# Kernel optimization log

Hardware: AMD Instinct MI355X
Metric: run time of the kernel (lower is better)

The kernel has to match this reference:

```python
import jax, jax.numpy as jnp
import numpy as np

N_NODES = 50000
NEG_SLOPE = 0.2


def gat_layer(x, src, dst, w_src, w_dst, att_src, att_dst, bias):
    """Single-head PyG-style GATConv (bipartite weights, same x for src/dst)."""
    xs = x @ w_src                      # [N, C] messages (source projection)
    xd = x @ w_dst                      # [N, C] destination projection
    a_s = xs @ att_src                  # [N] per-node src attention logit
    a_d = xd @ att_dst                  # [N] per-node dst attention logit
    e = jax.nn.leaky_relu(a_s[src] + a_d[dst], NEG_SLOPE)   # [E]
    # segment softmax over edges grouped by destination node
    m = jax.ops.segment_max(e, dst, num_segments=N_NODES)    # [N]
    ex = jnp.exp(e - m[dst])
    denom = jax.ops.segment_sum(ex, dst, num_segments=N_NODES)  # [N]
    alpha = ex / denom[dst]             # [E]
    out = jax.ops.segment_sum(alpha[:, None] * xs[src], dst, num_segments=N_NODES)
    return out + bias


def setup_inputs() -> dict:
    key = jax.random.key(0)
    ks = jax.random.split(key, 12)
    d_in, hid, out = 256, 128, 128
    inv = lambda d: 1.0 / np.sqrt(d)
    x = jax.random.normal(ks[0], (N_NODES, d_in), dtype=jnp.float32)
    edge_index = jax.random.randint(ks[1], (2, 800000), 0, N_NODES, dtype=jnp.int32)
    return {
        "x": x,
        "edge_index": edge_index,
        "w1_src": jax.random.normal(ks[2], (d_in, hid), jnp.float32) * inv(d_in),
        "w1_dst": jax.random.normal(ks[3], (d_in, hid), jnp.float32) * inv(d_in),
        "att1_src": jax.random.normal(ks[4], (hid,), jnp.float32) * inv(hid),
        "att1_dst": jax.random.normal(ks[5], (hid,), jnp.float32) * inv(hid),
        "b1": jnp.zeros((hid,), jnp.float32),
        "w2_src": jax.random.normal(ks[6], (hid, out), jnp.float32) * inv(hid),
        "w2_dst": jax.random.normal(ks[7], (hid, out), jnp.float32) * inv(hid),
        "att2_src": jax.random.normal(ks[8], (out,), jnp.float32) * inv(out),
        "att2_dst": jax.random.normal(ks[9], (out,), jnp.float32) * inv(out),
        "b2": jnp.zeros((out,), jnp.float32),
    }


def reference(x, edge_index, w1_src, w1_dst, att1_src, att1_dst, b1,
              w2_src, w2_dst, att2_src, att2_dst, b2):
    # add self loops once (GATConv default add_self_loops=True)
    loop = jnp.arange(N_NODES, dtype=edge_index.dtype)
    src = jnp.concatenate([edge_index[0], loop])
    dst = jnp.concatenate([edge_index[1], loop])
    h = gat_layer(x, src, dst, w1_src, w1_dst, att1_src, att1_dst, b1)
    h = jax.nn.relu(h)
    return gat_layer(h, src, dst, w2_src, w2_dst, att2_src, att2_dst, b2)
```

## Files before the change

kernel.cpp:

```cpp
#include <hip/hip_runtime.h>

#define NN 50000
#define MAXD 64
#define NEG_SLOPE 0.2f

typedef _Float16 half8 __attribute__((ext_vector_type(8)));
typedef _Float16 half2v __attribute__((ext_vector_type(2)));
typedef float floatx4 __attribute__((ext_vector_type(4)));


__global__ __launch_bounds__(256) void mega_kernel(
    const int* __restrict__ src, const int* __restrict__ dst,
    int* cnt, int* seg, int e, int G_SCAT,
    const float* __restrict__ w1s, const float* __restrict__ a1s,
    const float* __restrict__ w1d, const float* __restrict__ a1d,
    const float* __restrict__ w2s, const float* __restrict__ a2s,
    const float* __restrict__ w2d, const float* __restrict__ a2d,
    float* u1, float* v1, float* u2, float* v2,
    const float* __restrict__ x, _Float16* __restrict__ C, int M, int G_GEMM) {
  constexpr int K = 256, KP = 72;
  __shared__ _Float16 Bt[128 * KP];
  int bid = blockIdx.x, tid = threadIdx.x;
  if (bid < G_SCAT) {
    int i0 = (bid * 256 + tid) * 8;
    int total = e + NN;
#pragma unroll
    for (int j = 0; j < 8; ++j) {
      int i = i0 + j;
      if (i < total) {
        int d, s;
        if (i < e) { d = dst[i]; s = src[i]; }
        else       { d = i - e;  s = d; }
        int r = atomicAdd(&cnt[d], 1);
        if (r < MAXD) seg[(size_t)d * MAXD + r] = s;
      }
    }
  } else if (bid < G_SCAT + 4) {
    int b = bid - G_SCAT;
    const float *w, *a;
    float* o;
    int d;
    if (b == 0) { w = w1s; a = a1s; o = u1; d = K; }
    else if (b == 1) { w = w1d; a = a1d; o = v1; d = K; }
    else if (b == 2) { w = w2s; a = a2s; o = u2; d = 128; }
    else { w = w2d; a = a2d; o = v2; d = 128; }
    if (tid < d) {
      float s = 0.f;
      for (int j = 0; j < 128; ++j) s += w[tid * 128 + j] * a[j];
      o[tid] = s;
    }
  } else {
    __builtin_amdgcn_s_setprio(1);
    int gb = bid - G_SCAT - 4;
    int lane = tid & 63, wave = tid >> 6;
    int row_base = gb * 64 + wave * 16;
    int lr = lane & 15, lk = lane >> 4;
    floatx4 acc[8];
#pragma unroll
    for (int q = 0; q < 8; ++q) acc[q] = {0.f, 0.f, 0.f, 0.f};
    for (int kc = 0; kc < K; kc += 64) {
      for (int idx = tid; idx < 128 * 64; idx += 256) {
        int k = idx >> 7, c = idx & 127;
        Bt[c * KP + k] = (_Float16)w1s[(size_t)(kc + k) * 128 + c];
      }
      __syncthreads();
#pragma unroll
      for (int k0 = 0; k0 < 64; k0 += 32) {
        int row = row_base + lr;
        half8 a = {0, 0, 0, 0, 0, 0, 0, 0};
        if (row < M) {
          const float* ap = x + (size_t)row * K + kc + k0 + lk * 8;
          float4 f0 = *reinterpret_cast<const float4*>(ap);
          float4 f1 = *reinterpret_cast<const float4*>(ap + 4);
          a = half8{(_Float16)f0.x, (_Float16)f0.y, (_Float16)f0.z, (_Float16)f0.w,
                    (_Float16)f1.x, (_Float16)f1.y, (_Float16)f1.z, (_Float16)f1.w};
        }
        half8 b[8];
#pragma unroll
        for (int q = 0; q < 8; ++q)
          b[q] = *reinterpret_cast<const half8*>(&Bt[(q * 16 + lr) * KP + k0 + lk * 8]);
#pragma unroll
        for (int q = 0; q < 8; ++q)
          acc[q] = __builtin_amdgcn_mfma_f32_16x16x32_f16(a, b[q], acc[q], 0, 0, 0);
      }
      __syncthreads();
    }
#pragma unroll
    for (int q = 0; q < 8; ++q)
#pragma unroll
      for (int r = 0; r < 4; ++r) {
        int row = row_base + lk * 4 + r;
        if (row < M) C[(size_t)row * 128 + q * 16 + lr] = (_Float16)acc[q][r];
      }
    __builtin_amdgcn_s_setprio(0);
  }
}

__global__ __launch_bounds__(256) void ls_kernel(
    const int* __restrict__ cnt, int* seg, int G_SORT,
    const float* __restrict__ x, const float* __restrict__ u,
    const float* __restrict__ v, float* a_s, float* a_d) {
  int bid = blockIdx.x, tid = threadIdx.x;
  if (bid < G_SORT) {
    int wid = bid * 4 + (tid >> 6);
    int lane = tid & 63;
    if (wid < NN) {
      int L = cnt[wid];
      L = L < MAXD ? L : MAXD;
      if (L > 1) {
        int* srow = seg + (size_t)wid * MAXD;
        int v2_ = (lane < L) ? srow[lane] : 0x7fffffff;
#pragma unroll
        for (int k = 2; k <= 64; k <<= 1) {
#pragma unroll
          for (int j = k >> 1; j > 0; j >>= 1) {
            int other = __shfl_xor(v2_, j);
            bool dir = ((lane & k) == 0);
            bool lower = ((lane & j) == 0);
            int mn = v2_ < other ? v2_ : other;
            int mx = v2_ < other ? other : v2_;
            v2_ = (dir == lower) ? mn : mx;
          }
        }
        if (lane < L) srow[lane] = v2_;
      }
    }
  } else {
    int wid = (bid - G_SORT) * 4 + (tid >> 6);
    int lane = tid & 63;
    if (wid >= NN) return;
    const float* xr = x + (size_t)wid * 256 + lane * 4;
    float4 xv = *reinterpret_cast<const float4*>(xr);
    float4 uu = *reinterpret_cast<const float4*>(u + lane * 4);
    float4 vv = *reinterpret_cast<const float4*>(v + lane * 4);
    float s1 = xv.x * uu.x + xv.y * uu.y + xv.z * uu.z + xv.w * uu.w;
    float s2 = xv.x * vv.x + xv.y * vv.y + xv.z * vv.z + xv.w * vv.w;
#pragma unroll
    for (int off = 32; off; off >>= 1) {
      s1 += __shfl_xor(s1, off);
      s2 += __shfl_xor(s2, off);
    }
    if (lane == 0) { a_s[wid] = s1; a_d[wid] = s2; }
  }
}

__global__ __launch_bounds__(256) void fused2_kernel(
    const _Float16* __restrict__ A, const float* __restrict__ B,
    _Float16* __restrict__ C, int M, int G_GEMM,
    const _Float16* __restrict__ xin, const float* __restrict__ u,
    const float* __restrict__ v, float* a_s, float* a_d) {
  constexpr int K = 128, KP = 72;
  __shared__ _Float16 Bt[128 * KP];
  int bid = blockIdx.x, tid = threadIdx.x;
  if (bid < G_GEMM) {
    __builtin_amdgcn_s_setprio(1);
    int lane = tid & 63, wave = tid >> 6;
    int row_base = bid * 64 + wave * 16;
    int lr = lane & 15, lk = lane >> 4;
    floatx4 acc[8];
#pragma unroll
    for (int q = 0; q < 8; ++q) acc[q] = {0.f, 0.f, 0.f, 0.f};
    for (int kc = 0; kc < K; kc += 64) {
      for (int idx = tid; idx < 128 * 64; idx += 256) {
        int k = idx >> 7, c = idx & 127;
        Bt[c * KP + k] = (_Float16)B[(size_t)(kc + k) * 128 + c];
      }
      __syncthreads();
#pragma unroll
      for (int k0 = 0; k0 < 64; k0 += 32) {
        int row = row_base + lr;
        half8 a = {0, 0, 0, 0, 0, 0, 0, 0};
        if (row < M) a = *reinterpret_cast<const half8*>(&A[(size_t)row * K + kc + k0 + lk * 8]);
        half8 b[8];
#pragma unroll
        for (int q = 0; q < 8; ++q)
          b[q] = *reinterpret_cast<const half8*>(&Bt[(q * 16 + lr) * KP + k0 + lk * 8]);
#pragma unroll
        for (int q = 0; q < 8; ++q)
          acc[q] = __builtin_amdgcn_mfma_f32_16x16x32_f16(a, b[q], acc[q], 0, 0, 0);
      }
      __syncthreads();
    }
#pragma unroll
    for (int q = 0; q < 8; ++q)
#pragma unroll
      for (int r = 0; r < 4; ++r) {
        int row = row_base + lk * 4 + r;
        if (row < M) C[(size_t)row * 128 + q * 16 + lr] = (_Float16)acc[q][r];
      }
    __builtin_amdgcn_s_setprio(0);
  } else {
    int wid = (bid - G_GEMM) * 4 + (tid >> 6);
    int lane = tid & 63;
    if (wid >= NN) return;
    float s1 = 0.f, s2 = 0.f;
    const half2v* xr = reinterpret_cast<const half2v*>(&xin[(size_t)wid * 128]);
    {
      int i = lane;
      half2v xv = xr[i];
      float x0 = (float)xv[0], x1 = (float)xv[1];
      s1 = x0 * u[2 * i] + x1 * u[2 * i + 1];
      s2 = x0 * v[2 * i] + x1 * v[2 * i + 1];
    }
#pragma unroll
    for (int off = 32; off; off >>= 1) {
      s1 += __shfl_xor(s1, off);
      s2 += __shfl_xor(s2, off);
    }
    if (lane == 0) { a_s[wid] = s1; a_d[wid] = s2; }
  }
}

template <int LAYER>
__global__ __launch_bounds__(256) void agg_kernel(const int* __restrict__ cnt,
                                                  const int* __restrict__ seg,
                                                  const float* __restrict__ a_s,
                                                  const float* __restrict__ a_d,
                                                  const _Float16* __restrict__ xs,
                                                  const float* __restrict__ bias,
                                                  void* __restrict__ outp, int n) {
  int wid = (blockIdx.x * blockDim.x + threadIdx.x) >> 6;
  int lane = threadIdx.x & 63;
  if (wid >= n) return;
  int g = lane >> 3, lr = lane & 7;
  int L = cnt[wid];
  L = L < MAXD ? L : MAXD;
  const int* srow = seg + (size_t)wid * MAXD;
  float ad = a_d[wid];

  float denom = 0.f;
  float acc[16];
#pragma unroll
  for (int j = 0; j < 16; ++j) acc[j] = 0.f;

  int i = g;
  int s_cur = (i < L) ? srow[i] : -1;
  int i2 = i + 8;
  int s_next = (i2 < L) ? srow[i2] : -1;
  half8 v_cur0, v_cur1;
  float as_cur = 0.f;
  if (s_cur >= 0) {
    const _Float16* pr = &xs[(size_t)s_cur * 128 + lr * 16];
    v_cur0 = *reinterpret_cast<const half8*>(pr);
    v_cur1 = *reinterpret_cast<const half8*>(pr + 8);
    as_cur = a_s[s_cur];
  }
  while (s_cur >= 0) {
    half8 v_nx0, v_nx1;
    float as_nx = 0.f;
    if (s_next >= 0) {
      const _Float16* pr = &xs[(size_t)s_next * 128 + lr * 16];
      v_nx0 = *reinterpret_cast<const half8*>(pr);
      v_nx1 = *reinterpret_cast<const half8*>(pr + 8);
      as_nx = a_s[s_next];
    }
    int i3 = i2 + 8;
    int s_nx2 = (i3 < L) ? srow[i3] : -1;

    float e = as_cur + ad;
    e = e > 0.f ? e : NEG_SLOPE * e;
    float w = __expf(e);
    denom += w;
#pragma unroll
    for (int j = 0; j < 8; ++j) {
      acc[j] += w * (float)v_cur0[j];
      acc[8 + j] += w * (float)v_cur1[j];
    }
    s_cur = s_next; v_cur0 = v_nx0; v_cur1 = v_nx1; as_cur = as_nx;
    s_next = s_nx2; i2 = i3;
  }
  denom += __shfl_xor(denom, 8);
  denom += __shfl_xor(denom, 16);
  denom += __shfl_xor(denom, 32);
#pragma unroll
  for (int j = 0; j < 16; ++j) {
    acc[j] += __shfl_xor(acc[j], 8);
    acc[j] += __shfl_xor(acc[j], 16);
    acc[j] += __shfl_xor(acc[j], 32);
  }
  if (g == 0) {
    float inv = 1.0f / denom;
    float o[16];
#pragma unroll
    for (int j = 0; j < 16; ++j) o[j] = acc[j] * inv + bias[lr * 16 + j];
    if (LAYER == 1) {
      half8 h0, h1;
#pragma unroll
      for (int j = 0; j < 8; ++j) {
        h0[j] = (_Float16)fmaxf(o[j], 0.f);
        h1[j] = (_Float16)fmaxf(o[8 + j], 0.f);
      }
      _Float16* op = &((_Float16*)outp)[(size_t)wid * 128 + lr * 16];
      *reinterpret_cast<half8*>(op) = h0;
      *reinterpret_cast<half8*>(op + 8) = h1;
    } else {
      float* op = &((float*)outp)[(size_t)wid * 128 + lr * 16];
#pragma unroll
      for (int q = 0; q < 4; ++q) {
        float4 f = make_float4(o[q * 4], o[q * 4 + 1], o[q * 4 + 2], o[q * 4 + 3]);
        *reinterpret_cast<float4*>(op + q * 4) = f;
      }
    }
  }
}

extern "C" void kernel_launch(void* const* d_in, const int* in_sizes, int n_in,
                              void* d_out, int out_size, void* d_ws, size_t ws_size,
                              hipStream_t stream) {
  const float* x        = (const float*)d_in[0];
  const int*   eidx     = (const int*)d_in[1];
  const float* w1_src   = (const float*)d_in[2];
  const float* w1_dst   = (const float*)d_in[3];
  const float* att1_src = (const float*)d_in[4];
  const float* att1_dst = (const float*)d_in[5];
  const float* b1       = (const float*)d_in[6];
  const float* w2_src   = (const float*)d_in[7];
  const float* w2_dst   = (const float*)d_in[8];
  const float* att2_src = (const float*)d_in[9];
  const float* att2_dst = (const float*)d_in[10];
  const float* b2       = (const float*)d_in[11];

  const int E = in_sizes[1] / 2;
  const int* src = eidx;
  const int* dst = eidx + E;

  _Float16* h_h = (_Float16*)d_out;
  float*    out = (float*)d_out;

  char* ws = (char*)d_ws;
  size_t off = 0;
  auto alloc = [&](size_t bytes) -> void* {
    void* p = ws + off;
    off = (off + bytes + 255) & ~(size_t)255;
    return p;
  };
  _Float16* xs_h = (_Float16*)alloc((size_t)NN * 128 * sizeof(_Float16));
  float* a_s     = (float*)alloc((size_t)NN * sizeof(float));
  float* a_d     = (float*)alloc((size_t)NN * sizeof(float));
  int*   cnt     = (int*)alloc((size_t)NN * sizeof(int));
  int*   seg     = (int*)alloc((size_t)NN * MAXD * sizeof(int));
  float* u1      = (float*)alloc(256 * sizeof(float));
  float* v1      = (float*)alloc(256 * sizeof(float));
  float* u2      = (float*)alloc(256 * sizeof(float));
  float* v2      = (float*)alloc(256 * sizeof(float));

  const int G_SCAT = ((E + NN) / 8 + 255) / 256;
  const int G_GEMM = (NN + 63) / 64;
  const int G_SORT = (NN + 3) / 4;
  const int G_LOG  = (NN + 3) / 4;
  const int wave_blocks = (NN * 64 + 255) / 256;

  hipMemsetAsync(cnt, 0, NN * sizeof(int), stream);

  mega_kernel<<<G_SCAT + 4 + G_GEMM, 256, 0, stream>>>(
      src, dst, cnt, seg, E, G_SCAT,
      w1_src, att1_src, w1_dst, att1_dst, w2_src, att2_src, w2_dst, att2_dst,
      u1, v1, u2, v2, x, xs_h, NN, G_GEMM);

  ls_kernel<<<G_SORT + G_LOG, 256, 0, stream>>>(cnt, seg, G_SORT, x, u1, v1, a_s, a_d);

  agg_kernel<1><<<wave_blocks, 256, 0, stream>>>(cnt, seg, a_s, a_d, xs_h, b1, h_h, NN);

  fused2_kernel<<<G_GEMM + G_LOG, 256, 0, stream>>>(
      h_h, w2_src, xs_h, NN, G_GEMM, h_h, u2, v2, a_s, a_d);

  agg_kernel<2><<<wave_blocks, 256, 0, stream>>>(cnt, seg, a_s, a_d, xs_h, b2, out, NN);
}
```

Before: 165.9 us.

## Fuse per-row sort into layer-1 aggregation and logits into mega kernel

Moves the attention-vector precompute and the cnt zeroing into a small init kernel that replaces the memset. The layer-1 logit dot products now run as extra blocks of the scatter/GEMM mega kernel. The bitonic sort of each destination's source list now happens inside the layer-1 aggregation wave, which keeps the sorted indices in registers and reads them by shuffle. This removes one launch and one pass over seg, at the cost of an extra launch for init and sort work on the aggregation critical path. It also drops the setprio hint on the GEMM blocks.

```diff
diff --git a/kernel.cpp b/kernel.cpp
--- a/kernel.cpp
+++ b/kernel.cpp
@@ -8,15 +8,39 @@
 typedef _Float16 half2v __attribute__((ext_vector_type(2)));
 typedef float floatx4 __attribute__((ext_vector_type(4)));
 
-
-__global__ __launch_bounds__(256) void mega_kernel(
-    const int* __restrict__ src, const int* __restrict__ dst,
-    int* cnt, int* seg, int e, int G_SCAT,
+__global__ __launch_bounds__(256) void init_kernel(
     const float* __restrict__ w1s, const float* __restrict__ a1s,
     const float* __restrict__ w1d, const float* __restrict__ a1d,
     const float* __restrict__ w2s, const float* __restrict__ a2s,
     const float* __restrict__ w2d, const float* __restrict__ a2d,
-    float* u1, float* v1, float* u2, float* v2,
+    float* u1, float* v1, float* u2, float* v2, int din, int* cnt) {
+  int b = blockIdx.x, tid = threadIdx.x;
+  if (b < 4) {
+    const float *w, *a;
+    float* o;
+    int d;
+    if (b == 0) { w = w1s; a = a1s; o = u1; d = din; }
+    else if (b == 1) { w = w1d; a = a1d; o = v1; d = din; }
+    else if (b == 2) { w = w2s; a = a2s; o = u2; d = 128; }
+    else { w = w2d; a = a2d; o = v2; d = 128; }
+    if (tid < d) {
+      float s = 0.f;
+      for (int j = 0; j < 128; ++j) s += w[tid * 128 + j] * a[j];
+      o[tid] = s;
+    }
+  } else {
+    int i = (b - 4) * 256 + tid;
+    if (i < NN) cnt[i] = 0;
+  }
+}
+
+
+__global__ __launch_bounds__(256) void mega_kernel(
+    const int* __restrict__ src, const int* __restrict__ dst,
+    int* cnt, int* seg, int e, int G_SCAT,
+    const float* __restrict__ w1s,
+    const float* __restrict__ u1, const float* __restrict__ v1,
+    float* a_s, float* a_d,
     const float* __restrict__ x, _Float16* __restrict__ C, int M, int G_GEMM) {
   constexpr int K = 256, KP = 72;
   __shared__ _Float16 Bt[128 * KP];
@@ -35,23 +59,8 @@
         if (r < MAXD) seg[(size_t)d * MAXD + r] = s;
       }
     }
-  } else if (bid < G_SCAT + 4) {
-    int b = bid - G_SCAT;
-    const float *w, *a;
-    float* o;
-    int d;
-    if (b == 0) { w = w1s; a = a1s; o = u1; d = K; }
-    else if (b == 1) { w = w1d; a = a1d; o = v1; d = K; }
-    else if (b == 2) { w = w2s; a = a2s; o = u2; d = 128; }
-    else { w = w2d; a = a2d; o = v2; d = 128; }
-    if (tid < d) {
-      float s = 0.f;
-      for (int j = 0; j < 128; ++j) s += w[tid * 128 + j] * a[j];
-      o[tid] = s;
-    }
-  } else {
-    __builtin_amdgcn_s_setprio(1);
-    int gb = bid - G_SCAT - 4;
+  } else if (bid < G_SCAT + G_GEMM) {
+    int gb = bid - G_SCAT;
     int lane = tid & 63, wave = tid >> 6;
     int row_base = gb * 64 + wave * 16;
     int lr = lane & 15, lk = lane >> 4;
@@ -92,47 +101,14 @@
         int row = row_base + lk * 4 + r;
         if (row < M) C[(size_t)row * 128 + q * 16 + lr] = (_Float16)acc[q][r];
       }
-    __builtin_amdgcn_s_setprio(0);
-  }
-}
-
-__global__ __launch_bounds__(256) void ls_kernel(
-    const int* __restrict__ cnt, int* seg, int G_SORT,
-    const float* __restrict__ x, const float* __restrict__ u,
-    const float* __restrict__ v, float* a_s, float* a_d) {
-  int bid = blockIdx.x, tid = threadIdx.x;
-  if (bid < G_SORT) {
-    int wid = bid * 4 + (tid >> 6);
-    int lane = tid & 63;
-    if (wid < NN) {
-      int L = cnt[wid];
-      L = L < MAXD ? L : MAXD;
-      if (L > 1) {
-        int* srow = seg + (size_t)wid * MAXD;
-        int v2_ = (lane < L) ? srow[lane] : 0x7fffffff;
-#pragma unroll
-        for (int k = 2; k <= 64; k <<= 1) {
-#pragma unroll
-          for (int j = k >> 1; j > 0; j >>= 1) {
-            int other = __shfl_xor(v2_, j);
-            bool dir = ((lane & k) == 0);
-            bool lower = ((lane & j) == 0);
-            int mn = v2_ < other ? v2_ : other;
-            int mx = v2_ < other ? other : v2_;
-            v2_ = (dir == lower) ? mn : mx;
-          }
-        }
-        if (lane < L) srow[lane] = v2_;
-      }
-    }
   } else {
-    int wid = (bid - G_SORT) * 4 + (tid >> 6);
+    int wid = (bid - G_SCAT - G_GEMM) * 4 + (tid >> 6);
     int lane = tid & 63;
     if (wid >= NN) return;
     const float* xr = x + (size_t)wid * 256 + lane * 4;
     float4 xv = *reinterpret_cast<const float4*>(xr);
-    float4 uu = *reinterpret_cast<const float4*>(u + lane * 4);
-    float4 vv = *reinterpret_cast<const float4*>(v + lane * 4);
+    float4 uu = *reinterpret_cast<const float4*>(u1 + lane * 4);
+    float4 vv = *reinterpret_cast<const float4*>(v1 + lane * 4);
     float s1 = xv.x * uu.x + xv.y * uu.y + xv.z * uu.z + xv.w * uu.w;
     float s2 = xv.x * vv.x + xv.y * vv.y + xv.z * vv.z + xv.w * vv.w;
 #pragma unroll
@@ -141,6 +117,106 @@
       s2 += __shfl_xor(s2, off);
     }
     if (lane == 0) { a_s[wid] = s1; a_d[wid] = s2; }
+  }
+}
+
+__global__ __launch_bounds__(256) void agg1_kernel(
+    const int* __restrict__ cnt, int* __restrict__ seg,
+    const float* __restrict__ a_s, const float* __restrict__ a_d,
+    const _Float16* __restrict__ xs, const float* __restrict__ bias,
+    _Float16* __restrict__ outp, int n) {
+  int wid = (blockIdx.x * blockDim.x + threadIdx.x) >> 6;
+  int lane = threadIdx.x & 63;
+  if (wid >= n) return;
+  int L = cnt[wid];
+  L = L < MAXD ? L : MAXD;
+  int* srow = seg + (size_t)wid * MAXD;
+
+  int v = (lane < L) ? srow[lane] : 0x7fffffff;
+#pragma unroll
+  for (int k = 2; k <= 64; k <<= 1) {
+#pragma unroll
+    for (int j = k >> 1; j > 0; j >>= 1) {
+      int other = __shfl_xor(v, j);
+      bool dir = ((lane & k) == 0);
+      bool lower = ((lane & j) == 0);
+      int mn = v < other ? v : other;
+      int mx = v < other ? other : v;
+      v = (dir == lower) ? mn : mx;
+    }
+  }
+  if (lane < L) srow[lane] = v;
+
+  int g = lane >> 3, lr = lane & 7;
+  float ad = a_d[wid];
+  float denom = 0.f;
+  float acc[16];
+#pragma unroll
+  for (int j = 0; j < 16; ++j) acc[j] = 0.f;
+
+  auto idx_at = [&](int s_) -> int {
+    int val = __shfl(v, s_ & 63);
+    return (s_ < L) ? val : -1;
+  };
+
+  int slot = g;
+  int s_cur = idx_at(slot);
+  int slot2 = slot + 8;
+  int s_next = idx_at(slot2);
+  half8 c0, c1;
+  float as_c = 0.f;
+  if (s_cur >= 0) {
+    const _Float16* pr = &xs[(size_t)s_cur * 128 + lr * 16];
+    c0 = *reinterpret_cast<const half8*>(pr);
+    c1 = *reinterpret_cast<const half8*>(pr + 8);
+    as_c = a_s[s_cur];
+  }
+  while (s_cur >= 0) {
+    half8 n0, n1;
+    float as_n = 0.f;
+    if (s_next >= 0) {
+      const _Float16* pr = &xs[(size_t)s_next * 128 + lr * 16];
+      n0 = *reinterpret_cast<const half8*>(pr);
+      n1 = *reinterpret_cast<const half8*>(pr + 8);
+      as_n = a_s[s_next];
+    }
+    int slot3 = slot2 + 8;
+    int s_nx2 = idx_at(slot3);
+
+    float e = as_c + ad;
+    e = e > 0.f ? e : NEG_SLOPE * e;
+    float w = __expf(e);
+    denom += w;
+#pragma unroll
+    for (int j = 0; j < 8; ++j) {
+      acc[j] += w * (float)c0[j];
+      acc[8 + j] += w * (float)c1[j];
+    }
+    s_cur = s_next; c0 = n0; c1 = n1; as_c = as_n;
+    s_next = s_nx2; slot2 = slot3;
+  }
+  denom += __shfl_xor(denom, 8);
+  denom += __shfl_xor(denom, 16);
+  denom += __shfl_xor(denom, 32);
+#pragma unroll
+  for (int j = 0; j < 16; ++j) {
+    acc[j] += __shfl_xor(acc[j], 8);
+    acc[j] += __shfl_xor(acc[j], 16);
+    acc[j] += __shfl_xor(acc[j], 32);
+  }
+  if (g == 0) {
+    float inv = 1.0f / denom;
+    half8 h0, h1;
+#pragma unroll
+    for (int j = 0; j < 8; ++j) {
+      float o0 = acc[j] * inv + bias[lr * 16 + j];
+      float o1 = acc[8 + j] * inv + bias[lr * 16 + 8 + j];
+      h0[j] = (_Float16)fmaxf(o0, 0.f);
+      h1[j] = (_Float16)fmaxf(o1, 0.f);
+    }
+    _Float16* op = &outp[(size_t)wid * 128 + lr * 16];
+    *reinterpret_cast<half8*>(op) = h0;
+    *reinterpret_cast<half8*>(op + 8) = h1;
   }
 }
 
@@ -193,7 +269,7 @@
     int wid = (bid - G_GEMM) * 4 + (tid >> 6);
     int lane = tid & 63;
     if (wid >= NN) return;
-    float s1 = 0.f, s2 = 0.f;
+    float s1, s2;
     const half2v* xr = reinterpret_cast<const half2v*>(&xin[(size_t)wid * 128]);
     {
       int i = lane;
@@ -211,14 +287,11 @@
   }
 }
 
-template <int LAYER>
-__global__ __launch_bounds__(256) void agg_kernel(const int* __restrict__ cnt,
-                                                  const int* __restrict__ seg,
-                                                  const float* __restrict__ a_s,
-                                                  const float* __restrict__ a_d,
-                                                  const _Float16* __restrict__ xs,
-                                                  const float* __restrict__ bias,
-                                                  void* __restrict__ outp, int n) {
+__global__ __launch_bounds__(256) void agg2_kernel(
+    const int* __restrict__ cnt, const int* __restrict__ seg,
+    const float* __restrict__ a_s, const float* __restrict__ a_d,
+    const _Float16* __restrict__ xs, const float* __restrict__ bias,
+    float* __restrict__ outp, int n) {
   int wid = (blockIdx.x * blockDim.x + threadIdx.x) >> 6;
   int lane = threadIdx.x & 63;
   if (wid >= n) return;
@@ -237,36 +310,36 @@
   int s_cur = (i < L) ? srow[i] : -1;
   int i2 = i + 8;
   int s_next = (i2 < L) ? srow[i2] : -1;
-  half8 v_cur0, v_cur1;
-  float as_cur = 0.f;
+  half8 c0, c1;
+  float as_c = 0.f;
   if (s_cur >= 0) {
     const _Float16* pr = &xs[(size_t)s_cur * 128 + lr * 16];
-    v_cur0 = *reinterpret_cast<const half8*>(pr);
-    v_cur1 = *reinterpret_cast<const half8*>(pr + 8);
-    as_cur = a_s[s_cur];
+    c0 = *reinterpret_cast<const half8*>(pr);
+    c1 = *reinterpret_cast<const half8*>(pr + 8);
+    as_c = a_s[s_cur];
   }
   while (s_cur >= 0) {
-    half8 v_nx0, v_nx1;
-    float as_nx = 0.f;
+    half8 n0, n1;
+    float as_n = 0.f;
     if (s_next >= 0) {
       const _Float16* pr = &xs[(size_t)s_next * 128 + lr * 16];
-      v_nx0 = *reinterpret_cast<const half8*>(pr);
-      v_nx1 = *reinterpret_cast<const half8*>(pr + 8);
-      as_nx = a_s[s_next];
+      n0 = *reinterpret_cast<const half8*>(pr);
+      n1 = *reinterpret_cast<const half8*>(pr + 8);
+      as_n = a_s[s_next];
     }
     int i3 = i2 + 8;
     int s_nx2 = (i3 < L) ? srow[i3] : -1;
 
-    float e = as_cur + ad;
+    float e = as_c + ad;
     e = e > 0.f ? e : NEG_SLOPE * e;
     float w = __expf(e);
     denom += w;
 #pragma unroll
     for (int j = 0; j < 8; ++j) {
-      acc[j] += w * (float)v_cur0[j];
-      acc[8 + j] += w * (float)v_cur1[j];
-    }
-    s_cur = s_next; v_cur0 = v_nx0; v_cur1 = v_nx1; as_cur = as_nx;
+      acc[j] += w * (float)c0[j];
+      acc[8 + j] += w * (float)c1[j];
+    }
+    s_cur = s_next; c0 = n0; c1 = n1; as_c = as_n;
     s_next = s_nx2; i2 = i3;
   }
   denom += __shfl_xor(denom, 8);
@@ -283,23 +356,11 @@
     float o[16];
 #pragma unroll
     for (int j = 0; j < 16; ++j) o[j] = acc[j] * inv + bias[lr * 16 + j];
-    if (LAYER == 1) {
-      half8 h0, h1;
-#pragma unroll
-      for (int j = 0; j < 8; ++j) {
-        h0[j] = (_Float16)fmaxf(o[j], 0.f);
-        h1[j] = (_Float16)fmaxf(o[8 + j], 0.f);
-      }
-      _Float16* op = &((_Float16*)outp)[(size_t)wid * 128 + lr * 16];
-      *reinterpret_cast<half8*>(op) = h0;
-      *reinterpret_cast<half8*>(op + 8) = h1;
-    } else {
-      float* op = &((float*)outp)[(size_t)wid * 128 + lr * 16];
-#pragma unroll
-      for (int q = 0; q < 4; ++q) {
-        float4 f = make_float4(o[q * 4], o[q * 4 + 1], o[q * 4 + 2], o[q * 4 + 3]);
-        *reinterpret_cast<float4*>(op + q * 4) = f;
-      }
+    float* op = &outp[(size_t)wid * 128 + lr * 16];
+#pragma unroll
+    for (int q = 0; q < 4; ++q) {
+      float4 f = make_float4(o[q * 4], o[q * 4 + 1], o[q * 4 + 2], o[q * 4 + 3]);
+      *reinterpret_cast<float4*>(op + q * 4) = f;
     }
   }
 }
@@ -321,6 +382,7 @@
   const float* b2       = (const float*)d_in[11];
 
   const int E = in_sizes[1] / 2;
+  const int DIN = in_sizes[0] / NN;
   const int* src = eidx;
   const int* dst = eidx + E;
 
@@ -346,23 +408,21 @@
 
   const int G_SCAT = ((E + NN) / 8 + 255) / 256;
   const int G_GEMM = (NN + 63) / 64;
-  const int G_SORT = (NN + 3) / 4;
   const int G_LOG  = (NN + 3) / 4;
   const int wave_blocks = (NN * 64 + 255) / 256;
 
-  hipMemsetAsync(cnt, 0, NN * sizeof(int), stream);
-
-  mega_kernel<<<G_SCAT + 4 + G_GEMM, 256, 0, stream>>>(
+  init_kernel<<<4 + (NN + 255) / 256, 256, 0, stream>>>(
+      w1_src, att1_src, w1_dst, att1_dst, w2_src, att2_src, w2_dst, att2_dst,
+      u1, v1, u2, v2, DIN, cnt);
+
+  mega_kernel<<<G_SCAT + G_GEMM + G_LOG, 256, 0, stream>>>(
       src, dst, cnt, seg, E, G_SCAT,
-      w1_src, att1_src, w1_dst, att1_dst, w2_src, att2_src, w2_dst, att2_dst,
-      u1, v1, u2, v2, x, xs_h, NN, G_GEMM);
-
-  ls_kernel<<<G_SORT + G_LOG, 256, 0, stream>>>(cnt, seg, G_SORT, x, u1, v1, a_s, a_d);
-
-  agg_kernel<1><<<wave_blocks, 256, 0, stream>>>(cnt, seg, a_s, a_d, xs_h, b1, h_h, NN);
+      w1_src, u1, v1, a_s, a_d, x, xs_h, NN, G_GEMM);
+
+  agg1_kernel<<<wave_blocks, 256, 0, stream>>>(cnt, seg, a_s, a_d, xs_h, b1, h_h, NN);
 
   fused2_kernel<<<G_GEMM + G_LOG, 256, 0, stream>>>(
       h_h, w2_src, xs_h, NN, G_GEMM, h_h, u2, v2, a_s, a_d);
 
-  agg_kernel<2><<<wave_blocks, 256, 0, stream>>>(cnt, seg, a_s, a_d, xs_h, b2, out, NN);
-}
+  agg2_kernel<<<wave_blocks, 256, 0, stream>>>(cnt, seg, a_s, a_d, xs_h, b2, out, NN);
+}
```

Result: no change. 169.1 us, median of 2 (+1.9%).
